# Optimization experiments

Measured on AMD Instinct MI355X. Metric: run time of the kernel, lower is better.

The kernel has to match this reference:

```python
import jax, jax.numpy as jnp
import numpy as np

ANCHORS = np.array([[10,13],[16,30],[33,23],[30,61],[62,45],[59,119],
                    [116,90],[156,198],[373,326]], dtype=np.float32)
MASKS = [[6,7,8],[3,4,5],[0,1,2]]
NUM_CLASSES = 80
INPUT = 416.0          # input_shape == image_shape (no letterbox correction needed)
CONF_THRES = 0.5
NMS_THRES = 0.3
TOPK = 300             # fixed candidate budget per image (pad/mask for jit)


def decode_level(feat, mask):
    """feat: [B, A*(5+C), H, W] -> [B, A*H*W, 5+C] normalized xywh+conf+cls."""
    B, _, H, W = feat.shape
    A = len(mask)
    t = feat.reshape(B, A, 5 + NUM_CLASSES, H, W).transpose(0, 1, 3, 4, 2)  # [B,A,H,W,85]
    gy, gx = jnp.meshgrid(jnp.arange(H, dtype=feat.dtype),
                          jnp.arange(W, dtype=feat.dtype), indexing='ij')
    anc = jnp.asarray(ANCHORS[np.array(mask)])                    # [A,2] in input pixels
    x = (jax.nn.sigmoid(t[..., 0]) + gx) / W
    y = (jax.nn.sigmoid(t[..., 1]) + gy) / H
    w = jnp.exp(t[..., 2]) * anc[:, 0][None, :, None, None] / INPUT
    h = jnp.exp(t[..., 3]) * anc[:, 1][None, :, None, None] / INPUT
    conf = jax.nn.sigmoid(t[..., 4])
    cls = jax.nn.sigmoid(t[..., 5:])
    out = jnp.concatenate([jnp.stack([x, y, w, h, conf], axis=-1), cls], axis=-1)
    return out.reshape(B, A * H * W, 5 + NUM_CLASSES)


def pairwise_iou(b):
    # b: [K,4] corner boxes
    area = (b[:, 2] - b[:, 0]) * (b[:, 3] - b[:, 1])
    lt = jnp.maximum(b[:, None, :2], b[None, :, :2])
    rb = jnp.minimum(b[:, None, 2:], b[None, :, 2:])
    wh = jnp.clip(rb - lt, 0.0)
    inter = wh[..., 0] * wh[..., 1]
    return inter / (area[:, None] + area[None, :] - inter + 1e-6)


def nms_image(pred):
    """pred: [N, 5+C] -> [TOPK, 6] = (x1,y1,x2,y2,score,class), zero-padded."""
    obj = pred[:, 4]
    cls_conf = jnp.max(pred[:, 5:], axis=-1)
    cls_id = jnp.argmax(pred[:, 5:], axis=-1)
    score = obj * cls_conf
    score = jnp.where(score >= CONF_THRES, score, 0.0)   # confidence filter (masked)
    score_top, idx = jax.lax.top_k(score, TOPK)
    xywh = pred[idx, :4]
    boxes = jnp.concatenate([xywh[:, :2] - xywh[:, 2:] * 0.5,
                             xywh[:, :2] + xywh[:, 2:] * 0.5], axis=-1) * INPUT
    cls_top = cls_id[idx]
    # class-aware NMS via coordinate offset trick
    off = cls_top.astype(boxes.dtype)[:, None] * (2.0 * INPUT)
    iou = pairwise_iou(boxes + off)
    ar = jnp.arange(TOPK)

    def body(i, keep):
        sup = (iou[i] > NMS_THRES) & (ar > i) & keep[i]
        return keep & ~sup

    keep = jax.lax.fori_loop(0, TOPK, body, jnp.ones(TOPK, dtype=bool))
    valid = keep & (score_top > 0.0)
    m = valid.astype(boxes.dtype)
    return jnp.concatenate([boxes * m[:, None],
                            (score_top * m)[:, None],
                            (cls_top.astype(boxes.dtype) * m)[:, None]], axis=-1)


def setup_inputs() -> dict:
    key = jax.random.key(0)
    k0, k1, k2 = jax.random.split(key, 3)
    B, C = 32, 3 * (5 + NUM_CLASSES)
    return {
        'feat0': jax.random.normal(k0, (B, C, 13, 13), dtype=jnp.float32),
        'feat1': jax.random.normal(k1, (B, C, 26, 26), dtype=jnp.float32),
        'feat2': jax.random.normal(k2, (B, C, 52, 52), dtype=jnp.float32),
    }


def reference(feat0, feat1, feat2):
    outputs = jnp.concatenate([
        decode_level(feat0, MASKS[0]),
        decode_level(feat1, MASKS[1]),
        decode_level(feat2, MASKS[2]),
    ], axis=1)                      # [B, 10647, 85]
    return jax.vmap(nms_image)(outputs)   # [B, TOPK, 6]
```

## Files before the change

### kernel.cpp

```cpp
#include <hip/hip_runtime.h>
#include <math.h>

#define NUM_CLASSES 80
#define TOPK 300
#define NTOT 10647
#define L0END 507
#define L1END 2535
#define SELCAP 2048

__constant__ float ANCWf[3][3] = {{116.f,156.f,373.f},{30.f,62.f,59.f},{10.f,16.f,33.f}};
__constant__ float ANCHf[3][3] = {{90.f,198.f,326.f},{61.f,45.f,119.f},{13.f,30.f,23.f}};

__device__ __forceinline__ float expcr(float x) { return (float)exp((double)x); }
__device__ __forceinline__ float sigf(float x) {
    float e = expcr(-x);
    return __fdiv_rn(1.0f, __fadd_rn(1.0f, e));
}

__device__ __forceinline__ const float* locate(const float* f0, const float* f1, const float* f2,
                                               int img, int idx,
                                               int& level, int& hw, int& W, int& hrow, int& wcol, int& a) {
    int local, cell;
    const float* base;
    if (idx < L0END) {
        level = 0; local = idx; hw = 169; W = 13;
        base = f0 + (size_t)img * 43095;
    } else if (idx < L1END) {
        level = 1; local = idx - L0END; hw = 676; W = 26;
        base = f1 + (size_t)img * 172380;
    } else {
        level = 2; local = idx - L1END; hw = 2704; W = 52;
        base = f2 + (size_t)img * 689520;
    }
    a = local / hw; cell = local - a * hw;
    hrow = cell / W; wcol = cell - hrow * W;
    return base + (size_t)(a * 85) * hw + cell;
}

__global__ void score_kernel(const float* __restrict__ f0, const float* __restrict__ f1,
                             const float* __restrict__ f2,
                             unsigned long long* __restrict__ keys) {
    int t = blockIdx.x * blockDim.x + threadIdx.x;

    if (t < 32 * 512) {
        int img = t >> 9;
        int r = t & 511;
        if (r < 507) {
            int a = r / 169, cell = r - a * 169;
            const float* p = f0 + (size_t)img * 43095 + (size_t)(a * 85) * 169 + cell;
            float obj = sigf(p[4 * 169]);
            float mx = p[5 * 169];
            #pragma unroll 16
            for (int c = 1; c < NUM_CLASSES; ++c) {
                float v = p[(5 + c) * 169];
                if (v > mx) mx = v;
            }
            float s = __fmul_rn(obj, sigf(mx));
            unsigned long long kv = 0ULL;
            if (s >= 0.5f)
                kv = ((unsigned long long)__float_as_uint(s) << 32) | (unsigned int)(~(unsigned int)r);
            keys[(size_t)img * NTOT + r] = kv;
        }
    } else if (t < 64 * 512) {
        int tt = t - 32 * 512;
        int img = tt >> 9;
        int r = tt & 511;
        if (r < 507) {
            int a = r / 169, grp = r - a * 169;
            int cell0 = grp * 4;
            const float* p0 = f1 + (size_t)img * 172380 + (size_t)(a * 85) * 676 + cell0;
            float4 o4 = *(const float4*)(p0 + 4 * 676);
            float4 mx = *(const float4*)(p0 + 5 * 676);
            #pragma unroll 16
            for (int c = 1; c < NUM_CLASSES; ++c) {
                float4 v = *(const float4*)(p0 + (5 + c) * 676);
                mx.x = fmaxf(mx.x, v.x); mx.y = fmaxf(mx.y, v.y);
                mx.z = fmaxf(mx.z, v.z); mx.w = fmaxf(mx.w, v.w);
            }
            float ob[4] = {o4.x, o4.y, o4.z, o4.w};
            float mv[4] = {mx.x, mx.y, mx.z, mx.w};
            unsigned long long* kout = keys + (size_t)img * NTOT + (L0END + a * 676 + cell0);
            #pragma unroll
            for (int j = 0; j < 4; ++j) {
                float s = __fmul_rn(sigf(ob[j]), sigf(mv[j]));
                unsigned int idx = L0END + a * 676 + cell0 + j;
                unsigned long long kv = 0ULL;
                if (s >= 0.5f)
                    kv = ((unsigned long long)__float_as_uint(s) << 32) | (unsigned int)(~idx);
                kout[j] = kv;
            }
        }
    } else {
        int tt = t - 64 * 512;
        int img = tt >> 11;
        int r = tt & 2047;
        if (r < 2028) {
            int a = r / 676, grp = r - a * 676;
            int cell0 = grp * 4;
            const float* p0 = f2 + (size_t)img * 689520 + (size_t)(a * 85) * 2704 + cell0;
            float4 o4 = *(const float4*)(p0 + 4 * 2704);
            float4 mx = *(const float4*)(p0 + 5 * 2704);
            #pragma unroll 16
            for (int c = 1; c < NUM_CLASSES; ++c) {
                float4 v = *(const float4*)(p0 + (5 + c) * 2704);
                mx.x = fmaxf(mx.x, v.x); mx.y = fmaxf(mx.y, v.y);
                mx.z = fmaxf(mx.z, v.z); mx.w = fmaxf(mx.w, v.w);
            }
            float ob[4] = {o4.x, o4.y, o4.z, o4.w};
            float mv[4] = {mx.x, mx.y, mx.z, mx.w};
            unsigned long long* kout = keys + (size_t)img * NTOT + (L1END + a * 2704 + cell0);
            #pragma unroll
            for (int j = 0; j < 4; ++j) {
                float s = __fmul_rn(sigf(ob[j]), sigf(mv[j]));
                unsigned int idx = L1END + a * 2704 + cell0 + j;
                unsigned long long kv = 0ULL;
                if (s >= 0.5f)
                    kv = ((unsigned long long)__float_as_uint(s) << 32) | (unsigned int)(~idx);
                kout[j] = kv;
            }
        }
    }
}

__global__ __launch_bounds__(1024) void topk_kernel(const unsigned long long* __restrict__ keys,
                                                    unsigned int* __restrict__ top_idx) {
    __shared__ unsigned long long s[NTOT];
    __shared__ unsigned int hist[1024];
    __shared__ unsigned long long sel[SELCAP];
    __shared__ unsigned int wsum[16], wsuf[16];
    __shared__ unsigned int cnt;
    __shared__ int Tbin;

    int img = blockIdx.x;
    int tid = threadIdx.x;
    int wv = tid >> 6, ln = tid & 63;
    const unsigned long long* k = keys + (size_t)img * NTOT;

    hist[tid] = 0;
    if (tid == 0) { cnt = 0; Tbin = 0; }
    for (int i = tid; i < TOPK; i += 1024) top_idx[img * TOPK + i] = 0xFFFFFFFFu;
    __syncthreads();

    for (int i = tid; i < NTOT; i += 1024) {
        unsigned long long kv = k[i];
        s[i] = kv;
        unsigned int sb = (unsigned int)(kv >> 32);
        int bin = (int)(sb - 0x3F000000u) >> 13;
        if (bin >= 0) {
            if (bin > 1023) bin = 1023;
            atomicAdd(&hist[bin], 1u);
        }
    }
    __syncthreads();

    unsigned int ssum = hist[tid];
    #pragma unroll
    for (int off = 1; off < 64; off <<= 1) {
        unsigned int o = __shfl_down(ssum, off, 64);
        if (ln + off < 64) ssum += o;
    }
    if (ln == 0) wsum[wv] = ssum;
    __syncthreads();
    if (wv == 0) {
        unsigned int tws = (ln < 16) ? wsum[ln] : 0u;
        #pragma unroll
        for (int off = 1; off < 16; off <<= 1) {
            unsigned int o = __shfl_down(tws, off, 64);
            if (ln + off < 16) tws += o;
        }
        if (ln < 16) wsuf[ln] = tws;
    }
    __syncthreads();
    unsigned int higher = (wv < 15) ? wsuf[wv + 1] : 0u;
    unsigned int scanval = ssum + higher;
    unsigned int down1 = __shfl_down(scanval, 1, 64);
    unsigned int nextval = (ln < 63) ? down1 : higher;
    if (scanval >= TOPK && nextval < TOPK) Tbin = tid;
    __syncthreads();
    int T = Tbin;

    for (int i = tid; i < NTOT; i += 1024) {
        unsigned long long kv = s[i];
        unsigned int sb = (unsigned int)(kv >> 32);
        int bin = (int)(sb - 0x3F000000u) >> 13;
        if (bin > 1023) bin = 1023;
        if (bin >= T) {
            unsigned int pos = atomicAdd(&cnt, 1u);
            if (pos < SELCAP) sel[pos] = kv;
        }
    }
    __syncthreads();
    int m = (int)cnt; if (m > SELCAP) m = SELCAP;

    for (int i = tid; i < m; i += 1024) {
        unsigned long long ki = sel[i];
        int rank = 0;
        for (int j = 0; j < m; ++j) rank += (sel[j] > ki);
        if (rank < TOPK) top_idx[img * TOPK + rank] = ~((unsigned int)ki);
    }
}

__global__ __launch_bounds__(256) void decode_top_kernel(const float* __restrict__ f0,
                                                         const float* __restrict__ f1,
                                                         const float* __restrict__ f2,
                                                         const unsigned int* __restrict__ top_idx,
                                                         float* __restrict__ rows, int nrows) {
    int gw = blockIdx.x * 4 + (threadIdx.x >> 6);
    int lane = threadIdx.x & 63;
    if (gw >= nrows) return;
    int img = gw / TOPK, k = gw - img * TOPK;
    float* row = rows + (size_t)gw * 8;
    unsigned int idx = top_idx[img * TOPK + k];
    if (idx == 0xFFFFFFFFu) {
        if (lane < 8) row[lane] = 0.0f;
        return;
    }
    int level, hw, W, hrow, wcol, a;
    const float* p = locate(f0, f1, f2, img, (int)idx, level, hw, W, hrow, wcol, a);

    float v1 = p[(5 + lane) * hw];
    float bestv = sigf(v1);
    int besti = lane;
    if (lane < 16) {
        float v2 = p[(69 + lane) * hw];
        float sv2 = sigf(v2);
        if (sv2 > bestv) { bestv = sv2; besti = 64 + lane; }
    }
    #pragma unroll
    for (int off = 32; off > 0; off >>= 1) {
        float ov = __shfl_xor(bestv, off, 64);
        int oi = __shfl_xor(besti, off, 64);
        if (ov > bestv || (ov == bestv && oi < besti)) { bestv = ov; besti = oi; }
    }

    float tval = (lane < 5) ? p[lane * hw] : 0.0f;
    float tx = __shfl(tval, 0, 64);
    float ty = __shfl(tval, 1, 64);
    float tw = __shfl(tval, 2, 64);
    float th = __shfl(tval, 3, 64);
    float tob = __shfl(tval, 4, 64);

    if (lane == 0) {
        float x = __fdiv_rn(__fadd_rn(sigf(tx), (float)wcol), (float)W);
        float y = __fdiv_rn(__fadd_rn(sigf(ty), (float)hrow), (float)W);
        float wd = __fdiv_rn(__fmul_rn(expcr(tw), ANCWf[level][a]), 416.0f);
        float ht = __fdiv_rn(__fmul_rn(expcr(th), ANCHf[level][a]), 416.0f);
        float obj = sigf(tob);
        float score = __fmul_rn(obj, bestv);
        if (!(score >= 0.5f)) score = 0.0f;

        float hx = __fmul_rn(wd, 0.5f);
        float hy = __fmul_rn(ht, 0.5f);
        float x1 = __fmul_rn(__fsub_rn(x, hx), 416.0f);
        float y1 = __fmul_rn(__fsub_rn(y, hy), 416.0f);
        float x2 = __fmul_rn(__fadd_rn(x, hx), 416.0f);
        float y2 = __fmul_rn(__fadd_rn(y, hy), 416.0f);

        row[0] = x1; row[1] = y1; row[2] = x2; row[3] = y2;
        row[4] = score; row[5] = (float)besti; row[6] = 0.0f; row[7] = 0.0f;
    }
}

__global__ __launch_bounds__(1024) void nms_core_kernel(const float* __restrict__ rows,
                                                        float* __restrict__ out) {
    __shared__ float bx0[TOPK], bx1[TOPK], bx2[TOPK], bx3[TOPK];
    __shared__ float bb0[TOPK], bb1[TOPK], bb2[TOPK], bb3[TOPK];
    __shared__ float area[TOPK], sc[TOPK], clsf[TOPK];
    __shared__ unsigned long long sup[TOPK][5];
    __shared__ unsigned long long keepm[5];

    int img = blockIdx.x;
    int tid = threadIdx.x;
    int wave = tid >> 6, lane = tid & 63;

    if (tid < TOPK) {
        const float* row = rows + ((size_t)img * TOPK + tid) * 8;
        float x1 = row[0], y1 = row[1], x2 = row[2], y2 = row[3];
        float score = row[4], cf = row[5];
        float off = __fmul_rn(cf, 832.0f);
        bx0[tid] = x1; bx1[tid] = y1; bx2[tid] = x2; bx3[tid] = y2;
        float b0 = __fadd_rn(x1, off), b1 = __fadd_rn(y1, off);
        float b2 = __fadd_rn(x2, off), b3 = __fadd_rn(y2, off);
        bb0[tid] = b0; bb1[tid] = b1; bb2[tid] = b2; bb3[tid] = b3;
        area[tid] = __fmul_rn(__fsub_rn(b2, b0), __fsub_rn(b3, b1));
        sc[tid] = score;
        clsf[tid] = cf;
    }
    __syncthreads();

    #pragma unroll
    for (int w = 0; w < 5; ++w) {
        int j = (w << 6) + lane;
        bool jv = (j < TOPK);
        float j0 = jv ? bb0[j] : 0.0f;
        float j1 = jv ? bb1[j] : 0.0f;
        float j2 = jv ? bb2[j] : 0.0f;
        float j3 = jv ? bb3[j] : 0.0f;
        float ja = jv ? area[j] : 0.0f;
        for (int r = wave; r < TOPK; r += 16) {
            float a0 = bb0[r], a1 = bb1[r], a2 = bb2[r], a3 = bb3[r], aa = area[r];
            bool bit = false;
            if (jv && j > r) {
                float ltx = fmaxf(a0, j0);
                float lty = fmaxf(a1, j1);
                float rbx = fminf(a2, j2);
                float rby = fminf(a3, j3);
                float wx = fmaxf(__fsub_rn(rbx, ltx), 0.0f);
                float wy = fmaxf(__fsub_rn(rby, lty), 0.0f);
                float inter = __fmul_rn(wx, wy);
                float denom = __fadd_rn(__fsub_rn(__fadd_rn(aa, ja), inter), 1e-6f);
                float iou = __fdiv_rn(inter, denom);
                bit = (iou > 0.3f);
            }
            unsigned long long m = __ballot(bit);
            if (lane == 0) sup[r][w] = m;
        }
    }
    __syncthreads();

    if (wave == 0) {
        unsigned long long kp = ~0ULL;
        for (int i = 0; i < TOPK; ++i) {
            unsigned long long kw = __shfl(kp, i >> 6, 64);
            bool keep_i = (kw >> (i & 63)) & 1ULL;
            if (keep_i && lane < 5) kp &= ~sup[i][lane];
        }
        if (lane < 5) keepm[lane] = kp;
    }
    __syncthreads();

    if (tid < TOPK) {
        bool kept = (keepm[tid >> 6] >> (tid & 63)) & 1ULL;
        float m = (kept && (sc[tid] > 0.0f)) ? 1.0f : 0.0f;
        float* o = out + ((size_t)img * TOPK + tid) * 6;
        o[0] = __fmul_rn(bx0[tid], m);
        o[1] = __fmul_rn(bx1[tid], m);
        o[2] = __fmul_rn(bx2[tid], m);
        o[3] = __fmul_rn(bx3[tid], m);
        o[4] = __fmul_rn(sc[tid], m);
        o[5] = __fmul_rn(clsf[tid], m);
    }
}

extern "C" void kernel_launch(void* const* d_in, const int* in_sizes, int n_in,
                              void* d_out, int out_size, void* d_ws, size_t ws_size,
                              hipStream_t stream) {
    const float* f0 = (const float*)d_in[0];
    const float* f1 = (const float*)d_in[1];
    const float* f2 = (const float*)d_in[2];
    float* out = (float*)d_out;

    int B = in_sizes[0] / 43095;
    int nrows = B * TOPK;

    unsigned int* top_idx = (unsigned int*)d_ws;
    size_t off1 = ((size_t)nrows * sizeof(unsigned int) + 255) / 256 * 256;
    float* rows = (float*)((char*)d_ws + off1);
    size_t off2 = off1 + ((size_t)nrows * 8 * sizeof(float) + 255) / 256 * 256;
    unsigned long long* keys = (unsigned long long*)((char*)d_ws + off2);

    score_kernel<<<98304 / 256, 256, 0, stream>>>(f0, f1, f2, keys);
    topk_kernel<<<B, 1024, 0, stream>>>(keys, top_idx);
    decode_top_kernel<<<(nrows + 3) / 4, 256, 0, stream>>>(f0, f1, f2, top_idx, rows, nrows);
    nms_core_kernel<<<B, 1024, 0, stream>>>(rows, out);
}
```

Before: 100.2 us.

## Fuse top-k, candidate decode and NMS into one per-image kernel

Merges the top-k selection, top-candidate decode and NMS kernels into a single per-image block kernel. Top indices and decoded boxes stay in shared memory instead of going through workspace buffers. This removes two kernel launches and their global round trips. In exchange the decode now runs on only B blocks of 16 waves rather than many small blocks, and shared memory use per block grows.

```diff
diff --git a/kernel.cpp b/kernel.cpp
--- a/kernel.cpp
+++ b/kernel.cpp
@@ -122,14 +122,23 @@
     }
 }
 
-__global__ __launch_bounds__(1024) void topk_kernel(const unsigned long long* __restrict__ keys,
-                                                    unsigned int* __restrict__ top_idx) {
+__global__ __launch_bounds__(1024) void topk_nms_kernel(const float* __restrict__ f0,
+                                                        const float* __restrict__ f1,
+                                                        const float* __restrict__ f2,
+                                                        const unsigned long long* __restrict__ keys,
+                                                        float* __restrict__ out) {
     __shared__ unsigned long long s[NTOT];
     __shared__ unsigned int hist[1024];
     __shared__ unsigned long long sel[SELCAP];
     __shared__ unsigned int wsum[16], wsuf[16];
     __shared__ unsigned int cnt;
     __shared__ int Tbin;
+    __shared__ unsigned int tidx[TOPK];
+    __shared__ float bx0[TOPK], bx1[TOPK], bx2[TOPK], bx3[TOPK];
+    __shared__ float bb0[TOPK], bb1[TOPK], bb2[TOPK], bb3[TOPK];
+    __shared__ float area[TOPK], sc[TOPK], clsf[TOPK];
+    __shared__ unsigned long long sup[TOPK][5];
+    __shared__ unsigned long long keepm[5];
 
     int img = blockIdx.x;
     int tid = threadIdx.x;
@@ -138,7 +147,7 @@
 
     hist[tid] = 0;
     if (tid == 0) { cnt = 0; Tbin = 0; }
-    for (int i = tid; i < TOPK; i += 1024) top_idx[img * TOPK + i] = 0xFFFFFFFFu;
+    for (int i = tid; i < TOPK; i += 1024) tidx[i] = 0xFFFFFFFFu;
     __syncthreads();
 
     for (int i = tid; i < NTOT; i += 1024) {
@@ -171,11 +180,13 @@
         if (ln < 16) wsuf[ln] = tws;
     }
     __syncthreads();
-    unsigned int higher = (wv < 15) ? wsuf[wv + 1] : 0u;
-    unsigned int scanval = ssum + higher;
-    unsigned int down1 = __shfl_down(scanval, 1, 64);
-    unsigned int nextval = (ln < 63) ? down1 : higher;
-    if (scanval >= TOPK && nextval < TOPK) Tbin = tid;
+    {
+        unsigned int higher = (wv < 15) ? wsuf[wv + 1] : 0u;
+        unsigned int scanval = ssum + higher;
+        unsigned int down1 = __shfl_down(scanval, 1, 64);
+        unsigned int nextval = (ln < 63) ? down1 : higher;
+        if (scanval >= TOPK && nextval < TOPK) Tbin = tid;
+    }
     __syncthreads();
     int T = Tbin;
 
@@ -196,108 +207,84 @@
         unsigned long long ki = sel[i];
         int rank = 0;
         for (int j = 0; j < m; ++j) rank += (sel[j] > ki);
-        if (rank < TOPK) top_idx[img * TOPK + rank] = ~((unsigned int)ki);
-    }
-}
-
-__global__ __launch_bounds__(256) void decode_top_kernel(const float* __restrict__ f0,
-                                                         const float* __restrict__ f1,
-                                                         const float* __restrict__ f2,
-                                                         const unsigned int* __restrict__ top_idx,
-                                                         float* __restrict__ rows, int nrows) {
-    int gw = blockIdx.x * 4 + (threadIdx.x >> 6);
-    int lane = threadIdx.x & 63;
-    if (gw >= nrows) return;
-    int img = gw / TOPK, k = gw - img * TOPK;
-    float* row = rows + (size_t)gw * 8;
-    unsigned int idx = top_idx[img * TOPK + k];
-    if (idx == 0xFFFFFFFFu) {
-        if (lane < 8) row[lane] = 0.0f;
-        return;
-    }
-    int level, hw, W, hrow, wcol, a;
-    const float* p = locate(f0, f1, f2, img, (int)idx, level, hw, W, hrow, wcol, a);
-
-    float v1 = p[(5 + lane) * hw];
-    float bestv = sigf(v1);
-    int besti = lane;
-    if (lane < 16) {
-        float v2 = p[(69 + lane) * hw];
-        float sv2 = sigf(v2);
-        if (sv2 > bestv) { bestv = sv2; besti = 64 + lane; }
-    }
-    #pragma unroll
-    for (int off = 32; off > 0; off >>= 1) {
-        float ov = __shfl_xor(bestv, off, 64);
-        int oi = __shfl_xor(besti, off, 64);
-        if (ov > bestv || (ov == bestv && oi < besti)) { bestv = ov; besti = oi; }
-    }
-
-    float tval = (lane < 5) ? p[lane * hw] : 0.0f;
-    float tx = __shfl(tval, 0, 64);
-    float ty = __shfl(tval, 1, 64);
-    float tw = __shfl(tval, 2, 64);
-    float th = __shfl(tval, 3, 64);
-    float tob = __shfl(tval, 4, 64);
-
-    if (lane == 0) {
-        float x = __fdiv_rn(__fadd_rn(sigf(tx), (float)wcol), (float)W);
-        float y = __fdiv_rn(__fadd_rn(sigf(ty), (float)hrow), (float)W);
-        float wd = __fdiv_rn(__fmul_rn(expcr(tw), ANCWf[level][a]), 416.0f);
-        float ht = __fdiv_rn(__fmul_rn(expcr(th), ANCHf[level][a]), 416.0f);
-        float obj = sigf(tob);
-        float score = __fmul_rn(obj, bestv);
-        if (!(score >= 0.5f)) score = 0.0f;
-
-        float hx = __fmul_rn(wd, 0.5f);
-        float hy = __fmul_rn(ht, 0.5f);
-        float x1 = __fmul_rn(__fsub_rn(x, hx), 416.0f);
-        float y1 = __fmul_rn(__fsub_rn(y, hy), 416.0f);
-        float x2 = __fmul_rn(__fadd_rn(x, hx), 416.0f);
-        float y2 = __fmul_rn(__fadd_rn(y, hy), 416.0f);
-
-        row[0] = x1; row[1] = y1; row[2] = x2; row[3] = y2;
-        row[4] = score; row[5] = (float)besti; row[6] = 0.0f; row[7] = 0.0f;
-    }
-}
-
-__global__ __launch_bounds__(1024) void nms_core_kernel(const float* __restrict__ rows,
-                                                        float* __restrict__ out) {
-    __shared__ float bx0[TOPK], bx1[TOPK], bx2[TOPK], bx3[TOPK];
-    __shared__ float bb0[TOPK], bb1[TOPK], bb2[TOPK], bb3[TOPK];
-    __shared__ float area[TOPK], sc[TOPK], clsf[TOPK];
-    __shared__ unsigned long long sup[TOPK][5];
-    __shared__ unsigned long long keepm[5];
-
-    int img = blockIdx.x;
-    int tid = threadIdx.x;
-    int wave = tid >> 6, lane = tid & 63;
-
-    if (tid < TOPK) {
-        const float* row = rows + ((size_t)img * TOPK + tid) * 8;
-        float x1 = row[0], y1 = row[1], x2 = row[2], y2 = row[3];
-        float score = row[4], cf = row[5];
-        float off = __fmul_rn(cf, 832.0f);
-        bx0[tid] = x1; bx1[tid] = y1; bx2[tid] = x2; bx3[tid] = y2;
-        float b0 = __fadd_rn(x1, off), b1 = __fadd_rn(y1, off);
-        float b2 = __fadd_rn(x2, off), b3 = __fadd_rn(y2, off);
-        bb0[tid] = b0; bb1[tid] = b1; bb2[tid] = b2; bb3[tid] = b3;
-        area[tid] = __fmul_rn(__fsub_rn(b2, b0), __fsub_rn(b3, b1));
-        sc[tid] = score;
-        clsf[tid] = cf;
+        if (rank < TOPK) tidx[rank] = ~((unsigned int)ki);
+    }
+    __syncthreads();
+
+    for (int kk = wv; kk < TOPK; kk += 16) {
+        unsigned int idx = tidx[kk];
+        if (idx == 0xFFFFFFFFu) {
+            if (ln == 0) {
+                bx0[kk] = 0.f; bx1[kk] = 0.f; bx2[kk] = 0.f; bx3[kk] = 0.f;
+                bb0[kk] = 0.f; bb1[kk] = 0.f; bb2[kk] = 0.f; bb3[kk] = 0.f;
+                area[kk] = 0.f; sc[kk] = 0.f; clsf[kk] = 0.f;
+            }
+        } else {
+            int level, hw, W, hrow, wcol, a;
+            const float* p = locate(f0, f1, f2, img, (int)idx, level, hw, W, hrow, wcol, a);
+
+            float v1 = p[(5 + ln) * hw];
+            float bestv = sigf(v1);
+            int besti = ln;
+            if (ln < 16) {
+                float v2 = p[(69 + ln) * hw];
+                float sv2 = sigf(v2);
+                if (sv2 > bestv) { bestv = sv2; besti = 64 + ln; }
+            }
+            #pragma unroll
+            for (int off = 32; off > 0; off >>= 1) {
+                float ov = __shfl_xor(bestv, off, 64);
+                int oi = __shfl_xor(besti, off, 64);
+                if (ov > bestv || (ov == bestv && oi < besti)) { bestv = ov; besti = oi; }
+            }
+
+            float tval = (ln < 5) ? p[ln * hw] : 0.0f;
+            float tx = __shfl(tval, 0, 64);
+            float ty = __shfl(tval, 1, 64);
+            float tw = __shfl(tval, 2, 64);
+            float th = __shfl(tval, 3, 64);
+            float tob = __shfl(tval, 4, 64);
+
+            if (ln == 0) {
+                float x = __fdiv_rn(__fadd_rn(sigf(tx), (float)wcol), (float)W);
+                float y = __fdiv_rn(__fadd_rn(sigf(ty), (float)hrow), (float)W);
+                float wd = __fdiv_rn(__fmul_rn(expcr(tw), ANCWf[level][a]), 416.0f);
+                float ht = __fdiv_rn(__fmul_rn(expcr(th), ANCHf[level][a]), 416.0f);
+                float obj = sigf(tob);
+                float score = __fmul_rn(obj, bestv);
+                if (!(score >= 0.5f)) score = 0.0f;
+
+                float hx = __fmul_rn(wd, 0.5f);
+                float hy = __fmul_rn(ht, 0.5f);
+                float x1 = __fmul_rn(__fsub_rn(x, hx), 416.0f);
+                float y1 = __fmul_rn(__fsub_rn(y, hy), 416.0f);
+                float x2 = __fmul_rn(__fadd_rn(x, hx), 416.0f);
+                float y2 = __fmul_rn(__fadd_rn(y, hy), 416.0f);
+                float cf = (float)besti;
+                float off2 = __fmul_rn(cf, 832.0f);
+
+                bx0[kk] = x1; bx1[kk] = y1; bx2[kk] = x2; bx3[kk] = y2;
+                float b0 = __fadd_rn(x1, off2), b1 = __fadd_rn(y1, off2);
+                float b2 = __fadd_rn(x2, off2), b3 = __fadd_rn(y2, off2);
+                bb0[kk] = b0; bb1[kk] = b1; bb2[kk] = b2; bb3[kk] = b3;
+                area[kk] = __fmul_rn(__fsub_rn(b2, b0), __fsub_rn(b3, b1));
+                sc[kk] = score;
+                clsf[kk] = cf;
+            }
+        }
     }
     __syncthreads();
 
     #pragma unroll
     for (int w = 0; w < 5; ++w) {
-        int j = (w << 6) + lane;
+        int j = (w << 6) + ln;
         bool jv = (j < TOPK);
         float j0 = jv ? bb0[j] : 0.0f;
         float j1 = jv ? bb1[j] : 0.0f;
         float j2 = jv ? bb2[j] : 0.0f;
         float j3 = jv ? bb3[j] : 0.0f;
         float ja = jv ? area[j] : 0.0f;
-        for (int r = wave; r < TOPK; r += 16) {
+        for (int r = wv; r < TOPK; r += 16) {
             float a0 = bb0[r], a1 = bb1[r], a2 = bb2[r], a3 = bb3[r], aa = area[r];
             bool bit = false;
             if (jv && j > r) {
@@ -312,33 +299,33 @@
                 float iou = __fdiv_rn(inter, denom);
                 bit = (iou > 0.3f);
             }
-            unsigned long long m = __ballot(bit);
-            if (lane == 0) sup[r][w] = m;
-        }
-    }
-    __syncthreads();
-
-    if (wave == 0) {
+            unsigned long long mm = __ballot(bit);
+            if (ln == 0) sup[r][w] = mm;
+        }
+    }
+    __syncthreads();
+
+    if (wv == 0) {
         unsigned long long kp = ~0ULL;
         for (int i = 0; i < TOPK; ++i) {
             unsigned long long kw = __shfl(kp, i >> 6, 64);
             bool keep_i = (kw >> (i & 63)) & 1ULL;
-            if (keep_i && lane < 5) kp &= ~sup[i][lane];
-        }
-        if (lane < 5) keepm[lane] = kp;
+            if (keep_i && ln < 5) kp &= ~sup[i][ln];
+        }
+        if (ln < 5) keepm[ln] = kp;
     }
     __syncthreads();
 
     if (tid < TOPK) {
         bool kept = (keepm[tid >> 6] >> (tid & 63)) & 1ULL;
-        float m = (kept && (sc[tid] > 0.0f)) ? 1.0f : 0.0f;
+        float mmask = (kept && (sc[tid] > 0.0f)) ? 1.0f : 0.0f;
         float* o = out + ((size_t)img * TOPK + tid) * 6;
-        o[0] = __fmul_rn(bx0[tid], m);
-        o[1] = __fmul_rn(bx1[tid], m);
-        o[2] = __fmul_rn(bx2[tid], m);
-        o[3] = __fmul_rn(bx3[tid], m);
-        o[4] = __fmul_rn(sc[tid], m);
-        o[5] = __fmul_rn(clsf[tid], m);
+        o[0] = __fmul_rn(bx0[tid], mmask);
+        o[1] = __fmul_rn(bx1[tid], mmask);
+        o[2] = __fmul_rn(bx2[tid], mmask);
+        o[3] = __fmul_rn(bx3[tid], mmask);
+        o[4] = __fmul_rn(sc[tid], mmask);
+        o[5] = __fmul_rn(clsf[tid], mmask);
     }
 }
 
@@ -351,16 +338,9 @@
     float* out = (float*)d_out;
 
     int B = in_sizes[0] / 43095;
-    int nrows = B * TOPK;
-
-    unsigned int* top_idx = (unsigned int*)d_ws;
-    size_t off1 = ((size_t)nrows * sizeof(unsigned int) + 255) / 256 * 256;
-    float* rows = (float*)((char*)d_ws + off1);
-    size_t off2 = off1 + ((size_t)nrows * 8 * sizeof(float) + 255) / 256 * 256;
-    unsigned long long* keys = (unsigned long long*)((char*)d_ws + off2);
+
+    unsigned long long* keys = (unsigned long long*)d_ws;
 
     score_kernel<<<98304 / 256, 256, 0, stream>>>(f0, f1, f2, keys);
-    topk_kernel<<<B, 1024, 0, stream>>>(keys, top_idx);
-    decode_top_kernel<<<(nrows + 3) / 4, 256, 0, stream>>>(f0, f1, f2, top_idx, rows, nrows);
-    nms_core_kernel<<<B, 1024, 0, stream>>>(rows, out);
-}
+    topk_nms_kernel<<<B, 1024, 0, stream>>>(f0, f1, f2, keys, out);
+}
```

New measurement: 150.4 us. +50.1%, slower.

## Compute class id in score kernel and fold box decode into NMS kernel

Applied to the files above, without the earlier changes.

The score kernel now also finds the argmax class for each candidate that passes the threshold, using a second scan that matches sigmoid-equal values to the max, and stores it as a byte. The separate decode_top kernel goes away: the NMS kernel reads the top-k indices, decodes the boxes from the raw features, and takes the score from the stored keys. This drops one launch and the intermediate rows buffer. In exchange, the score kernel rescans class logits for passing cells, and the NMS kernel does scattered feature loads on only 300 threads.

```diff
diff --git a/kernel.cpp b/kernel.cpp
--- a/kernel.cpp
+++ b/kernel.cpp
@@ -7,6 +7,8 @@
 #define L0END 507
 #define L1END 2535
 #define SELCAP 2048
+#define CSTR 10656
+#define DELTA 0.25f
 
 __constant__ float ANCWf[3][3] = {{116.f,156.f,373.f},{30.f,62.f,59.f},{10.f,16.f,33.f}};
 __constant__ float ANCHf[3][3] = {{90.f,198.f,326.f},{61.f,45.f,119.f},{13.f,30.f,23.f}};
@@ -39,7 +41,8 @@
 
 __global__ void score_kernel(const float* __restrict__ f0, const float* __restrict__ f1,
                              const float* __restrict__ f2,
-                             unsigned long long* __restrict__ keys) {
+                             unsigned long long* __restrict__ keys,
+                             unsigned char* __restrict__ cls8) {
     int t = blockIdx.x * blockDim.x + threadIdx.x;
 
     if (t < 32 * 512) {
@@ -55,11 +58,20 @@
                 float v = p[(5 + c) * 169];
                 if (v > mx) mx = v;
             }
-            float s = __fmul_rn(obj, sigf(mx));
+            float smax = sigf(mx);
+            float s = __fmul_rn(obj, smax);
             unsigned long long kv = 0ULL;
             if (s >= 0.5f)
                 kv = ((unsigned long long)__float_as_uint(s) << 32) | (unsigned int)(~(unsigned int)r);
             keys[(size_t)img * NTOT + r] = kv;
+            if (s >= 0.5f) {
+                int cls = 0;
+                for (int c = 0; c < NUM_CLASSES; ++c) {
+                    float v = p[(5 + c) * 169];
+                    if (v >= mx - DELTA && sigf(v) == smax) { cls = c; break; }
+                }
+                cls8[(size_t)img * CSTR + r] = (unsigned char)cls;
+            }
         }
     } else if (t < 64 * 512) {
         int tt = t - 32 * 512;
@@ -70,24 +82,46 @@
             int cell0 = grp * 4;
             const float* p0 = f1 + (size_t)img * 172380 + (size_t)(a * 85) * 676 + cell0;
             float4 o4 = *(const float4*)(p0 + 4 * 676);
-            float4 mx = *(const float4*)(p0 + 5 * 676);
+            float4 mx4 = *(const float4*)(p0 + 5 * 676);
             #pragma unroll 16
             for (int c = 1; c < NUM_CLASSES; ++c) {
                 float4 v = *(const float4*)(p0 + (5 + c) * 676);
-                mx.x = fmaxf(mx.x, v.x); mx.y = fmaxf(mx.y, v.y);
-                mx.z = fmaxf(mx.z, v.z); mx.w = fmaxf(mx.w, v.w);
+                mx4.x = fmaxf(mx4.x, v.x); mx4.y = fmaxf(mx4.y, v.y);
+                mx4.z = fmaxf(mx4.z, v.z); mx4.w = fmaxf(mx4.w, v.w);
             }
             float ob[4] = {o4.x, o4.y, o4.z, o4.w};
-            float mv[4] = {mx.x, mx.y, mx.z, mx.w};
+            float mv[4] = {mx4.x, mx4.y, mx4.z, mx4.w};
+            float smaxv[4]; bool need[4];
             unsigned long long* kout = keys + (size_t)img * NTOT + (L0END + a * 676 + cell0);
             #pragma unroll
             for (int j = 0; j < 4; ++j) {
-                float s = __fmul_rn(sigf(ob[j]), sigf(mv[j]));
+                smaxv[j] = sigf(mv[j]);
+                float s = __fmul_rn(sigf(ob[j]), smaxv[j]);
                 unsigned int idx = L0END + a * 676 + cell0 + j;
                 unsigned long long kv = 0ULL;
                 if (s >= 0.5f)
                     kv = ((unsigned long long)__float_as_uint(s) << 32) | (unsigned int)(~idx);
                 kout[j] = kv;
+                need[j] = (s >= 0.5f);
+            }
+            if (need[0] || need[1] || need[2] || need[3]) {
+                int clsv[4] = {0, 0, 0, 0};
+                bool done[4] = {!need[0], !need[1], !need[2], !need[3]};
+                for (int c = 0; c < NUM_CLASSES; ++c) {
+                    float4 v = *(const float4*)(p0 + (5 + c) * 676);
+                    float vv[4] = {v.x, v.y, v.z, v.w};
+                    #pragma unroll
+                    for (int j = 0; j < 4; ++j) {
+                        if (!done[j] && vv[j] >= mv[j] - DELTA && sigf(vv[j]) == smaxv[j]) {
+                            clsv[j] = c; done[j] = true;
+                        }
+                    }
+                    if (done[0] && done[1] && done[2] && done[3]) break;
+                }
+                size_t cb = (size_t)img * CSTR + 512 + a * 676 + cell0;
+                #pragma unroll
+                for (int j = 0; j < 4; ++j)
+                    if (need[j]) cls8[cb + j] = (unsigned char)clsv[j];
             }
         }
     } else {
@@ -99,24 +133,46 @@
             int cell0 = grp * 4;
             const float* p0 = f2 + (size_t)img * 689520 + (size_t)(a * 85) * 2704 + cell0;
             float4 o4 = *(const float4*)(p0 + 4 * 2704);
-            float4 mx = *(const float4*)(p0 + 5 * 2704);
+            float4 mx4 = *(const float4*)(p0 + 5 * 2704);
             #pragma unroll 16
             for (int c = 1; c < NUM_CLASSES; ++c) {
                 float4 v = *(const float4*)(p0 + (5 + c) * 2704);
-                mx.x = fmaxf(mx.x, v.x); mx.y = fmaxf(mx.y, v.y);
-                mx.z = fmaxf(mx.z, v.z); mx.w = fmaxf(mx.w, v.w);
+                mx4.x = fmaxf(mx4.x, v.x); mx4.y = fmaxf(mx4.y, v.y);
+                mx4.z = fmaxf(mx4.z, v.z); mx4.w = fmaxf(mx4.w, v.w);
             }
             float ob[4] = {o4.x, o4.y, o4.z, o4.w};
-            float mv[4] = {mx.x, mx.y, mx.z, mx.w};
+            float mv[4] = {mx4.x, mx4.y, mx4.z, mx4.w};
+            float smaxv[4]; bool need[4];
             unsigned long long* kout = keys + (size_t)img * NTOT + (L1END + a * 2704 + cell0);
             #pragma unroll
             for (int j = 0; j < 4; ++j) {
-                float s = __fmul_rn(sigf(ob[j]), sigf(mv[j]));
+                smaxv[j] = sigf(mv[j]);
+                float s = __fmul_rn(sigf(ob[j]), smaxv[j]);
                 unsigned int idx = L1END + a * 2704 + cell0 + j;
                 unsigned long long kv = 0ULL;
                 if (s >= 0.5f)
                     kv = ((unsigned long long)__float_as_uint(s) << 32) | (unsigned int)(~idx);
                 kout[j] = kv;
+                need[j] = (s >= 0.5f);
+            }
+            if (need[0] || need[1] || need[2] || need[3]) {
+                int clsv[4] = {0, 0, 0, 0};
+                bool done[4] = {!need[0], !need[1], !need[2], !need[3]};
+                for (int c = 0; c < NUM_CLASSES; ++c) {
+                    float4 v = *(const float4*)(p0 + (5 + c) * 2704);
+                    float vv[4] = {v.x, v.y, v.z, v.w};
+                    #pragma unroll
+                    for (int j = 0; j < 4; ++j) {
+                        if (!done[j] && vv[j] >= mv[j] - DELTA && sigf(vv[j]) == smaxv[j]) {
+                            clsv[j] = c; done[j] = true;
+                        }
+                    }
+                    if (done[0] && done[1] && done[2] && done[3]) break;
+                }
+                size_t cb = (size_t)img * CSTR + 2540 + a * 2704 + cell0;
+                #pragma unroll
+                for (int j = 0; j < 4; ++j)
+                    if (need[j]) cls8[cb + j] = (unsigned char)clsv[j];
             }
         }
     }
@@ -171,11 +227,13 @@
         if (ln < 16) wsuf[ln] = tws;
     }
     __syncthreads();
-    unsigned int higher = (wv < 15) ? wsuf[wv + 1] : 0u;
-    unsigned int scanval = ssum + higher;
-    unsigned int down1 = __shfl_down(scanval, 1, 64);
-    unsigned int nextval = (ln < 63) ? down1 : higher;
-    if (scanval >= TOPK && nextval < TOPK) Tbin = tid;
+    {
+        unsigned int higher = (wv < 15) ? wsuf[wv + 1] : 0u;
+        unsigned int scanval = ssum + higher;
+        unsigned int down1 = __shfl_down(scanval, 1, 64);
+        unsigned int nextval = (ln < 63) ? down1 : higher;
+        if (scanval >= TOPK && nextval < TOPK) Tbin = tid;
+    }
     __syncthreads();
     int T = Tbin;
 
@@ -200,69 +258,13 @@
     }
 }
 
-__global__ __launch_bounds__(256) void decode_top_kernel(const float* __restrict__ f0,
-                                                         const float* __restrict__ f1,
-                                                         const float* __restrict__ f2,
-                                                         const unsigned int* __restrict__ top_idx,
-                                                         float* __restrict__ rows, int nrows) {
-    int gw = blockIdx.x * 4 + (threadIdx.x >> 6);
-    int lane = threadIdx.x & 63;
-    if (gw >= nrows) return;
-    int img = gw / TOPK, k = gw - img * TOPK;
-    float* row = rows + (size_t)gw * 8;
-    unsigned int idx = top_idx[img * TOPK + k];
-    if (idx == 0xFFFFFFFFu) {
-        if (lane < 8) row[lane] = 0.0f;
-        return;
-    }
-    int level, hw, W, hrow, wcol, a;
-    const float* p = locate(f0, f1, f2, img, (int)idx, level, hw, W, hrow, wcol, a);
-
-    float v1 = p[(5 + lane) * hw];
-    float bestv = sigf(v1);
-    int besti = lane;
-    if (lane < 16) {
-        float v2 = p[(69 + lane) * hw];
-        float sv2 = sigf(v2);
-        if (sv2 > bestv) { bestv = sv2; besti = 64 + lane; }
-    }
-    #pragma unroll
-    for (int off = 32; off > 0; off >>= 1) {
-        float ov = __shfl_xor(bestv, off, 64);
-        int oi = __shfl_xor(besti, off, 64);
-        if (ov > bestv || (ov == bestv && oi < besti)) { bestv = ov; besti = oi; }
-    }
-
-    float tval = (lane < 5) ? p[lane * hw] : 0.0f;
-    float tx = __shfl(tval, 0, 64);
-    float ty = __shfl(tval, 1, 64);
-    float tw = __shfl(tval, 2, 64);
-    float th = __shfl(tval, 3, 64);
-    float tob = __shfl(tval, 4, 64);
-
-    if (lane == 0) {
-        float x = __fdiv_rn(__fadd_rn(sigf(tx), (float)wcol), (float)W);
-        float y = __fdiv_rn(__fadd_rn(sigf(ty), (float)hrow), (float)W);
-        float wd = __fdiv_rn(__fmul_rn(expcr(tw), ANCWf[level][a]), 416.0f);
-        float ht = __fdiv_rn(__fmul_rn(expcr(th), ANCHf[level][a]), 416.0f);
-        float obj = sigf(tob);
-        float score = __fmul_rn(obj, bestv);
-        if (!(score >= 0.5f)) score = 0.0f;
-
-        float hx = __fmul_rn(wd, 0.5f);
-        float hy = __fmul_rn(ht, 0.5f);
-        float x1 = __fmul_rn(__fsub_rn(x, hx), 416.0f);
-        float y1 = __fmul_rn(__fsub_rn(y, hy), 416.0f);
-        float x2 = __fmul_rn(__fadd_rn(x, hx), 416.0f);
-        float y2 = __fmul_rn(__fadd_rn(y, hy), 416.0f);
-
-        row[0] = x1; row[1] = y1; row[2] = x2; row[3] = y2;
-        row[4] = score; row[5] = (float)besti; row[6] = 0.0f; row[7] = 0.0f;
-    }
-}
-
-__global__ __launch_bounds__(1024) void nms_core_kernel(const float* __restrict__ rows,
-                                                        float* __restrict__ out) {
+__global__ __launch_bounds__(1024) void nms_kernel(const float* __restrict__ f0,
+                                                   const float* __restrict__ f1,
+                                                   const float* __restrict__ f2,
+                                                   const unsigned long long* __restrict__ keys,
+                                                   const unsigned char* __restrict__ cls8,
+                                                   const unsigned int* __restrict__ top_idx,
+                                                   float* __restrict__ out) {
     __shared__ float bx0[TOPK], bx1[TOPK], bx2[TOPK], bx3[TOPK];
     __shared__ float bb0[TOPK], bb1[TOPK], bb2[TOPK], bb3[TOPK];
     __shared__ float area[TOPK], sc[TOPK], clsf[TOPK];
@@ -271,33 +273,61 @@
 
     int img = blockIdx.x;
     int tid = threadIdx.x;
-    int wave = tid >> 6, lane = tid & 63;
+    int wv = tid >> 6, ln = tid & 63;
 
     if (tid < TOPK) {
-        const float* row = rows + ((size_t)img * TOPK + tid) * 8;
-        float x1 = row[0], y1 = row[1], x2 = row[2], y2 = row[3];
-        float score = row[4], cf = row[5];
-        float off = __fmul_rn(cf, 832.0f);
-        bx0[tid] = x1; bx1[tid] = y1; bx2[tid] = x2; bx3[tid] = y2;
-        float b0 = __fadd_rn(x1, off), b1 = __fadd_rn(y1, off);
-        float b2 = __fadd_rn(x2, off), b3 = __fadd_rn(y2, off);
-        bb0[tid] = b0; bb1[tid] = b1; bb2[tid] = b2; bb3[tid] = b3;
-        area[tid] = __fmul_rn(__fsub_rn(b2, b0), __fsub_rn(b3, b1));
-        sc[tid] = score;
-        clsf[tid] = cf;
+        unsigned int idx = top_idx[img * TOPK + tid];
+        if (idx == 0xFFFFFFFFu) {
+            bx0[tid] = 0.f; bx1[tid] = 0.f; bx2[tid] = 0.f; bx3[tid] = 0.f;
+            bb0[tid] = 0.f; bb1[tid] = 0.f; bb2[tid] = 0.f; bb3[tid] = 0.f;
+            area[tid] = 0.f; sc[tid] = 0.f; clsf[tid] = 0.f;
+        } else {
+            int level, hw, W, hrow, wcol, a;
+            const float* p = locate(f0, f1, f2, img, (int)idx, level, hw, W, hrow, wcol, a);
+            float tx = p[0];
+            float ty = p[hw];
+            float tw = p[2 * hw];
+            float th = p[3 * hw];
+            float score = __uint_as_float((unsigned int)(keys[(size_t)img * NTOT + idx] >> 32));
+            int co = (idx < L0END) ? (int)idx
+                     : (idx < L1END ? 512 + (int)idx - L0END : 2540 + (int)idx - L1END);
+            int cid = cls8[(size_t)img * CSTR + co];
+
+            float x = __fdiv_rn(__fadd_rn(sigf(tx), (float)wcol), (float)W);
+            float y = __fdiv_rn(__fadd_rn(sigf(ty), (float)hrow), (float)W);
+            float wd = __fdiv_rn(__fmul_rn(expcr(tw), ANCWf[level][a]), 416.0f);
+            float ht = __fdiv_rn(__fmul_rn(expcr(th), ANCHf[level][a]), 416.0f);
+
+            float hx = __fmul_rn(wd, 0.5f);
+            float hy = __fmul_rn(ht, 0.5f);
+            float x1 = __fmul_rn(__fsub_rn(x, hx), 416.0f);
+            float y1 = __fmul_rn(__fsub_rn(y, hy), 416.0f);
+            float x2 = __fmul_rn(__fadd_rn(x, hx), 416.0f);
+            float y2 = __fmul_rn(__fadd_rn(y, hy), 416.0f);
+            float cf = (float)cid;
+            float off = __fmul_rn(cf, 832.0f);
+
+            bx0[tid] = x1; bx1[tid] = y1; bx2[tid] = x2; bx3[tid] = y2;
+            float b0 = __fadd_rn(x1, off), b1 = __fadd_rn(y1, off);
+            float b2 = __fadd_rn(x2, off), b3 = __fadd_rn(y2, off);
+            bb0[tid] = b0; bb1[tid] = b1; bb2[tid] = b2; bb3[tid] = b3;
+            area[tid] = __fmul_rn(__fsub_rn(b2, b0), __fsub_rn(b3, b1));
+            sc[tid] = score;
+            clsf[tid] = cf;
+        }
     }
     __syncthreads();
 
     #pragma unroll
     for (int w = 0; w < 5; ++w) {
-        int j = (w << 6) + lane;
+        int j = (w << 6) + ln;
         bool jv = (j < TOPK);
         float j0 = jv ? bb0[j] : 0.0f;
         float j1 = jv ? bb1[j] : 0.0f;
         float j2 = jv ? bb2[j] : 0.0f;
         float j3 = jv ? bb3[j] : 0.0f;
         float ja = jv ? area[j] : 0.0f;
-        for (int r = wave; r < TOPK; r += 16) {
+        for (int r = wv; r < TOPK; r += 16) {
             float a0 = bb0[r], a1 = bb1[r], a2 = bb2[r], a3 = bb3[r], aa = area[r];
             bool bit = false;
             if (jv && j > r) {
@@ -312,20 +342,20 @@
                 float iou = __fdiv_rn(inter, denom);
                 bit = (iou > 0.3f);
             }
-            unsigned long long m = __ballot(bit);
-            if (lane == 0) sup[r][w] = m;
-        }
-    }
-    __syncthreads();
-
-    if (wave == 0) {
+            unsigned long long mm = __ballot(bit);
+            if (ln == 0) sup[r][w] = mm;
+        }
+    }
+    __syncthreads();
+
+    if (wv == 0) {
         unsigned long long kp = ~0ULL;
         for (int i = 0; i < TOPK; ++i) {
             unsigned long long kw = __shfl(kp, i >> 6, 64);
             bool keep_i = (kw >> (i & 63)) & 1ULL;
-            if (keep_i && lane < 5) kp &= ~sup[i][lane];
-        }
-        if (lane < 5) keepm[lane] = kp;
+            if (keep_i && ln < 5) kp &= ~sup[i][ln];
+        }
+        if (ln < 5) keepm[ln] = kp;
     }
     __syncthreads();
 
@@ -351,16 +381,14 @@
     float* out = (float*)d_out;
 
     int B = in_sizes[0] / 43095;
-    int nrows = B * TOPK;
-
-    unsigned int* top_idx = (unsigned int*)d_ws;
-    size_t off1 = ((size_t)nrows * sizeof(unsigned int) + 255) / 256 * 256;
-    float* rows = (float*)((char*)d_ws + off1);
-    size_t off2 = off1 + ((size_t)nrows * 8 * sizeof(float) + 255) / 256 * 256;
-    unsigned long long* keys = (unsigned long long*)((char*)d_ws + off2);
-
-    score_kernel<<<98304 / 256, 256, 0, stream>>>(f0, f1, f2, keys);
+
+    unsigned long long* keys = (unsigned long long*)d_ws;
+    size_t off1 = (size_t)B * NTOT * sizeof(unsigned long long);
+    unsigned char* cls8 = (unsigned char*)d_ws + off1;
+    size_t off2 = (off1 + (size_t)B * CSTR + 255) / 256 * 256;
+    unsigned int* top_idx = (unsigned int*)((char*)d_ws + off2);
+
+    score_kernel<<<98304 / 256, 256, 0, stream>>>(f0, f1, f2, keys, cls8);
     topk_kernel<<<B, 1024, 0, stream>>>(keys, top_idx);
-    decode_top_kernel<<<(nrows + 3) / 4, 256, 0, stream>>>(f0, f1, f2, top_idx, rows, nrows);
-    nms_core_kernel<<<B, 1024, 0, stream>>>(rows, out);
-}
+    nms_kernel<<<B, 1024, 0, stream>>>(f0, f1, f2, keys, cls8, top_idx, out);
+}
```

Result: slower. 149.0 us (+48.7%).
